# Kernel tuning notes

Hardware: AMD Instinct MI355X
Metric: run time of the kernel (lower is better)

## Reference

```python
import jax, jax.numpy as jnp
import numpy as np

S, T, D_OUT = 64, 256, 64
B = 64
HEADS = 2
D0 = S + T              # 320
D1 = D0 * (1 + HEADS)   # 960
D2 = D1 * (1 + HEADS)   # 2880
PARAM_SCALE = 0.02


def setup_inputs() -> dict:
    key = jax.random.key(0)
    k1, k2, k3, k4 = jax.random.split(key, 4)
    x = jax.random.normal(k1, (B, T, S), dtype=jnp.float32)
    A0 = jax.random.normal(k2, (HEADS, D0, D0), dtype=jnp.float32) * PARAM_SCALE
    A1 = jax.random.normal(k3, (HEADS, D1, D1), dtype=jnp.float32) * PARAM_SCALE
    Wo = jax.random.normal(k4, (D_OUT, D2), dtype=jnp.float32) * PARAM_SCALE
    return {"x": x, "A0": A0, "A1": A1, "Wo": Wo}


def _causal_self_attention(h, A):
    # h: [B, T, d], A: [H, d, d]
    Bsz, Tlen, d = h.shape
    H = A.shape[0]
    # bilinear scores per head: h @ A[i] @ h^T, vectorized over heads
    scores = jnp.einsum('btd,hde,bse->bhts', h, A, h)  # [B, H, T, T]
    neg_inf = jnp.asarray(float('-inf'), dtype=h.dtype)
    mask = jnp.triu(jnp.full((Tlen, Tlen), neg_inf, dtype=h.dtype), k=1)
    attn = jax.nn.softmax(scores + mask, axis=-1)
    out = jnp.einsum('bhts,bsd->bthd', attn, h)  # [B, T, H, d]
    return out.reshape(Bsz, Tlen, H * d)


def reference(x, A0, A1, Wo):
    Bsz, Tlen, _ = x.shape
    # one-hot positional encoding concatenated onto input
    pos = jnp.broadcast_to(jnp.eye(Tlen, dtype=x.dtype)[None], (Bsz, Tlen, Tlen))
    h = jnp.concatenate([x, pos], axis=-1)          # [B, T, S+T]
    h = jnp.concatenate([h, _causal_self_attention(h, A0)], axis=-1)  # [B, T, D1]
    h = jnp.concatenate([h, _causal_self_attention(h, A1)], axis=-1)  # [B, T, D2]
    logits = jnp.einsum('btd,od->bto', h, Wo)       # [B, T, d_out]
    return logits
```

## Files before the change

kernel.cpp:

```cpp
#include <hip/hip_runtime.h>
#include <math.h>

#define NB 64
#define NT 256
#define NS 64
#define ND0 320
#define ND1 960
#define ND2 2880
#define NH 2
#define DC 704

typedef __attribute__((ext_vector_type(8))) _Float16 f16x8;
typedef __attribute__((ext_vector_type(4))) float f32x4;
typedef __attribute__((ext_vector_type(4))) short short4v;

typedef const __attribute__((address_space(1))) void* gas_ptr;
typedef __attribute__((address_space(3))) void* las_ptr;
#define GLOAD16(g, l) __builtin_amdgcn_global_load_lds((gas_ptr)(g), (las_ptr)(l), 16, 0, 0)
#define MFMAH(a, b, c) __builtin_amdgcn_mfma_f32_16x16x32_f16((a), (b), (c), 0, 0, 0)

__device__ __forceinline__ short f2h(float v) {
    union { _Float16 h; short s; } u; u.h = (_Float16)v; return u.s;
}
__device__ __forceinline__ float h2f(short b) {
    union { _Float16 h; short s; } u; u.s = b; return (float)u.h;
}
__device__ __forceinline__ int swz(int o) { return o ^ (((o >> 7) & 7) << 4); }

__global__ __launch_bounds__(256, 2) void gemmG1(
    const short* __restrict__ hc,
    const short* __restrict__ At,
    short* __restrict__ G,
    const float* __restrict__ A1)
{
    int wg = blockIdx.x;
    int q8 = gridDim.x >> 3;
    int sid = (wg & 7) * q8 + (wg >> 3);
    int bx = sid % 15, by = sid / 15;
    int m0 = by << 8, n0 = bx << 7;

    __shared__ short lds[24576];
    int tid = threadIdx.x;
    int lane = tid & 63, w = tid >> 6;
    int wm = w >> 1, wn = w & 1;
    int q = lane >> 4, l15 = lane & 15;

    const short* aS[4]; const short* bS[2];
    int dA[4], dB[2];
#pragma unroll
    for (int j = 0; j < 4; ++j) {
        int o = j * 4096 + tid * 16;
        int c = swz(o);
        int sr = c >> 7, byt = c & 127;
        int row = sr * 2 + (byt >> 6), k = (byt & 63) >> 1;
        aS[j] = hc + (long)(m0 + row) * DC + k;
        dA[j] = o >> 1;
    }
#pragma unroll
    for (int j = 0; j < 2; ++j) {
        int o = j * 4096 + tid * 16;
        int c = swz(o);
        int sr = c >> 7, byt = c & 127;
        int row = sr * 2 + (byt >> 6), k = (byt & 63) >> 1;
        bS[j] = At + (long)(n0 + row) * DC + k;
        dB[j] = o >> 1;
    }

#define STG(BUF) { \
    GLOAD16(aS[0], lds + (BUF) + dA[0]); GLOAD16(aS[1], lds + (BUF) + dA[1]); \
    GLOAD16(aS[2], lds + (BUF) + dA[2]); GLOAD16(aS[3], lds + (BUF) + dA[3]); \
    GLOAD16(bS[0], lds + (BUF) + 8192 + dB[0]); GLOAD16(bS[1], lds + (BUF) + 8192 + dB[1]); \
    aS[0] += 32; aS[1] += 32; aS[2] += 32; aS[3] += 32; bS[0] += 32; bS[1] += 32; }

    int oa[8], ob[4];
#pragma unroll
    for (int mf = 0; mf < 8; ++mf) {
        int row = wm * 128 + mf * 16 + l15;
        int sr = row >> 1, half = row & 1;
        oa[mf] = swz(sr * 128 + half * 64 + q * 16) >> 1;
    }
#pragma unroll
    for (int nf = 0; nf < 4; ++nf) {
        int row = wn * 64 + nf * 16 + l15;
        int sr = row >> 1, half = row & 1;
        ob[nf] = swz(sr * 128 + half * 64 + q * 16) >> 1;
    }

    f32x4 acc[8][4] = {};

    STG(0)
    __syncthreads();
#pragma unroll 2
    for (int t = 0; t < 22; ++t) {
        int cur = (t & 1) * 12288;
        if (t < 21) STG(12288 - cur)
        f16x8 vb[4];
#pragma unroll
        for (int nf = 0; nf < 4; ++nf)
            vb[nf] = *(const f16x8*)(lds + cur + 8192 + ob[nf]);
#pragma unroll
        for (int mf = 0; mf < 8; ++mf) {
            f16x8 va = *(const f16x8*)(lds + cur + oa[mf]);
#pragma unroll
            for (int nf = 0; nf < 4; ++nf)
                acc[mf][nf] = MFMAH(va, vb[nf], acc[mf][nf]);
        }
        __syncthreads();
    }
#undef STG

#pragma unroll
    for (int mf = 0; mf < 8; ++mf)
#pragma unroll
        for (int nf = 0; nf < 4; ++nf) {
            int col = n0 + wn * 64 + nf * 16 + l15;
            int head = (col >= 960) ? 1 : 0;
            int colh = col - head * 960;
            const float* bA = A1 + (long)head * 921600 + colh;
            int rowb = m0 + wm * 128 + mf * 16 + (q << 2);
#pragma unroll
            for (int r = 0; r < 4; ++r) {
                int t = (rowb + r) & 255;
                float f = acc[mf][nf][r] + bA[(long)(64 + t) * 960];
                G[(long)(rowb + r) * 1920 + col] = f2h(f);
            }
        }
}

template <bool AJUMP>
__global__ __launch_bounds__(256, 3) void gemm128(
    const short* Ah, int lda, long sA,
    const short* Bh, int ldb, long sB,
    short* Sf, int ldcf, long sCf,
    const short* biasH, long ldbias,
    long hsA, long hsC,
    int K)
{
    int bx = blockIdx.x, by = blockIdx.y;
    int m0 = by * 128, n0 = bx * 128;
    if (n0 > m0 + 127) return;
    long zLo = blockIdx.z & 63, zHi = blockIdx.z >> 6;
    const short* pAh = Ah + zLo * sA + zHi * hsA;
    const short* pBh = Bh + zLo * sB;

    __shared__ short lds[16384];
    short* LAh = lds;
    short* LBh = lds + 8192;

    int tid = threadIdx.x;
    int lane = tid & 63, w = tid >> 6;
    int wr = w >> 1, wc = w & 1;

    const short* aSH[4]; const short* bSH[4];
    int aLo[4], bLo[4];
#pragma unroll
    for (int j = 0; j < 4; ++j) {
        int o = j * 4096 + tid * 16;
        int c = swz(o); int r = c >> 7, col = (c & 127) >> 1;
        aSH[j] = pAh + (long)(m0 + r) * lda + col;
        aLo[j] = o >> 1;
        bSH[j] = pBh + (long)(n0 + r) * ldb + col;
        bLo[j] = o >> 1;
    }

    int oa[4][2], ob[4][2];
#pragma unroll
    for (int mf = 0; mf < 4; ++mf)
#pragma unroll
        for (int kf = 0; kf < 2; ++kf) {
            int row = wr * 64 + mf * 16 + (lane & 15);
            oa[mf][kf] = swz(row * 128 + (kf * 32 + ((lane >> 4) << 3)) * 2) >> 1;
        }
#pragma unroll
    for (int nf = 0; nf < 4; ++nf)
#pragma unroll
        for (int kf = 0; kf < 2; ++kf) {
            int row = wc * 64 + nf * 16 + (lane & 15);
            ob[nf][kf] = swz(row * 128 + (kf * 32 + ((lane >> 4) << 3)) * 2) >> 1;
        }

    f32x4 acc[4][4] = {};

    for (int k0 = 0; k0 < K; k0 += 64) {
        int step = (AJUMP && k0 == 0) ? 320 : 64;
#pragma unroll
        for (int j = 0; j < 4; ++j) {
            GLOAD16(aSH[j], LAh + aLo[j]);
            aSH[j] += step;
            GLOAD16(bSH[j], LBh + bLo[j]);
            bSH[j] += 64;
        }
        __syncthreads();
#pragma unroll
        for (int kf = 0; kf < 2; ++kf) {
            f16x8 vbh[4];
#pragma unroll
            for (int nf = 0; nf < 4; ++nf)
                vbh[nf] = *(const f16x8*)(LBh + ob[nf][kf]);
#pragma unroll
            for (int mf = 0; mf < 4; ++mf) {
                f16x8 vah = *(const f16x8*)(LAh + oa[mf][kf]);
#pragma unroll
                for (int nf = 0; nf < 4; ++nf)
                    acc[mf][nf] = MFMAH(vah, vbh[nf], acc[mf][nf]);
            }
        }
        __syncthreads();
    }

#pragma unroll
    for (int mf = 0; mf < 4; ++mf)
#pragma unroll
        for (int nf = 0; nf < 4; ++nf) {
            f32x4 v = acc[mf][nf];
            int col  = n0 + wc * 64 + nf * 16 + (lane & 15);
            int rowb = m0 + wr * 64 + mf * 16 + ((lane >> 4) << 2);
#pragma unroll
            for (int r = 0; r < 4; ++r) {
                long o = (zLo * 256 + rowb + r) * ldbias + 64 + col + zHi * hsA;
                v[r] += h2f(biasH[o]);
            }
#pragma unroll
            for (int r = 0; r < 4; ++r)
                Sf[zLo * sCf + zHi * hsC + (long)(rowb + r) * ldcf + col] = f2h(v[r]);
        }
}

template <int BMODE, bool KCAUSAL, bool ACC, bool OUTU, bool BJUMP>
__global__ __launch_bounds__(256) void gemm_mfma(
    const short* Ah, int lda, long sA,
    const short* Bh, int ldb, long sB, long hsB,
    float* Cf, int ldcf, long sCf,
    short* Chi, int ldch, long sCh,
    const float* biasF, long ldbias, long hsBias,
    long hsA, long hsC,
    short* UThi,
    int K)
{
    int m0 = blockIdx.y * 128, n0 = blockIdx.x * 64;
    long zLo = blockIdx.z & 63, zHi = blockIdx.z >> 6;
    const short* pAh = Ah + zLo * sA + zHi * hsA;
    const short* pBh = Bh + zLo * sB + zHi * hsB;

    __shared__ short lds[12288];
    short* LAh = lds;
    short* LBh = lds + 8192;

    int tid = threadIdx.x;
    int lane = tid & 63, w = tid >> 6;
    int wr = w >> 1, wc = w & 1;

    const short* aSH[4]; const short* bSH[2];
    int aLo[4], bLo[2];
#pragma unroll
    for (int j = 0; j < 4; ++j) {
        int o = j * 4096 + tid * 16;
        int c = swz(o); int r = c >> 7, col = (c & 127) >> 1;
        aSH[j] = pAh + (long)(m0 + r) * lda + col;
        aLo[j] = o >> 1;
    }
#pragma unroll
    for (int j = 0; j < 2; ++j) {
        int o = j * 4096 + tid * 16;
        int c = swz(o); int r = c >> 7, col = (c & 127) >> 1;
        bSH[j] = pBh + (long)(n0 + r) * ldb + col;
        bLo[j] = o >> 1;
    }

    int oa[4][2], ob[2][2];
#pragma unroll
    for (int mf = 0; mf < 4; ++mf)
#pragma unroll
        for (int kf = 0; kf < 2; ++kf) {
            int row = wr * 64 + mf * 16 + (lane & 15);
            oa[mf][kf] = swz(row * 128 + (kf * 32 + ((lane >> 4) << 3)) * 2) >> 1;
        }
#pragma unroll
    for (int nf = 0; nf < 2; ++nf)
#pragma unroll
        for (int kf = 0; kf < 2; ++kf) {
            int row = wc * 32 + nf * 16 + (lane & 15);
            ob[nf][kf] = swz(row * 128 + (kf * 32 + ((lane >> 4) << 3)) * 2) >> 1;
        }

    f32x4 acc[4][2] = {};
    int Klim = KCAUSAL ? (K < m0 + 128 ? K : m0 + 128) : K;

    for (int k0 = 0; k0 < Klim; k0 += 64) {
#pragma unroll
        for (int j = 0; j < 4; ++j) {
            GLOAD16(aSH[j], LAh + aLo[j]);
            aSH[j] += 64;
        }
        long bstep = (BJUMP && k0 == 192) ? (1048576L - 192L) : 64L;
#pragma unroll
        for (int j = 0; j < 2; ++j) {
            GLOAD16(bSH[j], LBh + bLo[j]);
            bSH[j] += bstep;
        }
        __syncthreads();
#pragma unroll
        for (int kf = 0; kf < 2; ++kf) {
            f16x8 vbh[2];
#pragma unroll
            for (int nf = 0; nf < 2; ++nf)
                vbh[nf] = *(const f16x8*)(LBh + ob[nf][kf]);
#pragma unroll
            for (int mf = 0; mf < 4; ++mf) {
                f16x8 vah = *(const f16x8*)(LAh + oa[mf][kf]);
#pragma unroll
                for (int nf = 0; nf < 2; ++nf)
                    acc[mf][nf] = MFMAH(vah, vbh[nf], acc[mf][nf]);
            }
        }
        __syncthreads();
    }

#pragma unroll
    for (int mf = 0; mf < 4; ++mf)
#pragma unroll
        for (int nf = 0; nf < 2; ++nf) {
            f32x4 v = acc[mf][nf];
            int col  = n0 + wc * 32 + nf * 16 + (lane & 15);
            int rowb = m0 + wr * 64 + mf * 16 + ((lane >> 4) << 2);
            if (BMODE == 1) {
#pragma unroll
                for (int r = 0; r < 4; ++r) {
                    int t = (rowb + r) & 255;
                    v[r] += biasF[zLo * hsBias + (long)(64 + t) * ldbias + col];
                }
            } else if (BMODE == 3) {
#pragma unroll
                for (int r = 0; r < 4; ++r) {
                    int t = (rowb + r) & 255;
                    v[r] += biasF[(long)(col - n0) * 2880 + (n0 >> 6) * 960 + 64 + t];
                }
            }
            if (OUTU) {
                if (n0 == 0) {
#pragma unroll
                    for (int r = 0; r < 4; ++r)
                        Cf[(long)(rowb + r) * ldcf + col] = v[r];
                } else {
                    int head = (n0 >> 6) - 1;
                    int o = col - n0;
                    short hs[4];
#pragma unroll
                    for (int r = 0; r < 4; ++r) hs[r] = f2h(v[r]);
                    short4v th = {hs[0], hs[1], hs[2], hs[3]};
                    *(short4v*)(UThi + head * 1048576L + (long)o * 16384 + rowb) = th;
                }
            } else if (ACC) {
#pragma unroll
                for (int r = 0; r < 4; ++r)
                    Cf[zLo * sCf + (long)(rowb + r) * ldcf + col] += v[r];
            } else if (Cf) {
#pragma unroll
                for (int r = 0; r < 4; ++r)
                    Cf[zLo * sCf + (long)(rowb + r) * ldcf + col] = v[r];
            } else {
#pragma unroll
                for (int r = 0; r < 4; ++r)
                    Chi[zHi * hsC + zLo * sCh + (long)(rowb + r) * ldch + col] = f2h(v[r]);
            }
        }
}

__global__ __launch_bounds__(256) void build_all(const float* __restrict__ x,
                                                 const float* __restrict__ Wo,
                                                 const float* __restrict__ A0,
                                                 short* __restrict__ hc,
                                                 short* __restrict__ hT,
                                                 short* __restrict__ Wf,
                                                 short* __restrict__ At0) {
    __shared__ float tile[32][33];
    int blk = blockIdx.x;
    int tid = threadIdx.x;
    if (blk < 4096) {
        int idx = blk * 256 + tid;
        int bt = idx >> 6, c = idx & 63;
        hc[(long)bt * DC + c] = f2h(x[(long)bt * NS + c]);
    } else if (blk < 5120) {
        int i = blk - 4096;
        int c0 = (i & 1) * 32, t0 = ((i >> 1) & 7) * 32, b = i >> 4;
        int tx = tid & 31, ty = tid >> 5;
        const float* xb = x + (long)b * NT * NS;
#pragma unroll
        for (int ii = ty; ii < 32; ii += 8) tile[ii][tx] = xb[(long)(t0 + ii) * NS + c0 + tx];
        __syncthreads();
        long base = (long)b * (NS * 256);
#pragma unroll
        for (int ii = ty; ii < 32; ii += 8)
            hT[base + (long)(c0 + ii) * 256 + t0 + tx] = f2h(tile[tx][ii]);
    } else if (blk < 5648) {
        int idx = (blk - 5120) * 256 + tid;
        if (idx < 192 * DC) {
            int r = idx / DC, kc = idx - r * DC;
            int o = r & 63, chunk = r >> 6;
            int srck = (kc < 64) ? kc : kc + 256;
            Wf[idx] = f2h(Wo[(long)o * ND2 + chunk * 960 + srck]);
        }
    } else {
        int i = blk - 5648;
        int k0 = (i & 1) * 32;
        int n0 = ((i >> 1) % 10) * 32;
        int z  = i / 20;
        int tx = tid & 31, ty = tid >> 5;
        long hbase = (long)z * ND0 * ND0;
#pragma unroll
        for (int ii = ty; ii < 32; ii += 8)
            tile[ii][tx] = A0[hbase + (long)(k0 + ii) * ND0 + n0 + tx];
        __syncthreads();
        long obase = (long)z * ND0 * 64;
#pragma unroll
        for (int ii = ty; ii < 32; ii += 8)
            At0[obase + (long)(n0 + ii) * 64 + k0 + tx] = f2h(tile[tx][ii]);
    }
}

__global__ void build_At(const float* __restrict__ A,
                         short* __restrict__ hi,
                         int dN, int dK, int srcLd, int shift, int dSrcN) {
    __shared__ float tile[32][33];
    int k0 = blockIdx.x * 32, n0 = blockIdx.y * 32;
    long hbase = (long)blockIdx.z * srcLd * srcLd;
    int tx = threadIdx.x, ty = threadIdx.y;
#pragma unroll
    for (int i = ty; i < 32; i += 8) {
        int k = k0 + i;
        int srck = (k < 64) ? k : k + shift;
        tile[i][tx] = (n0 + tx < dSrcN) ? A[hbase + (long)srck * srcLd + n0 + tx] : 0.f;
    }
    __syncthreads();
    long obase = (long)blockIdx.z * dN * dK;
#pragma unroll
    for (int i = ty; i < 32; i += 8)
        hi[obase + (long)(n0 + i) * dK + k0 + tx] = f2h(tile[tx][i]);
}

__global__ __launch_bounds__(256) void softmax_split(const short* S,
                                                     short* pHi,
                                                     int ldo, long hs) {
    int row  = blockIdx.x * 4 + (threadIdx.x >> 6);
    int t    = row & (NT - 1);
    int hrow = row & 16383;
    int head = row >> 14;
    int lane = threadIdx.x & 63;
    int s0   = lane << 2;
    const short* p = S + (long)row * NT;

    short4v sv = *(const short4v*)(p + s0);
    float vv[4] = {h2f(sv[0]), h2f(sv[1]), h2f(sv[2]), h2f(sv[3])};
    float mx = -INFINITY;
#pragma unroll
    for (int j = 0; j < 4; ++j)
        if (s0 + j <= t) mx = fmaxf(mx, vv[j]);
    for (int off = 32; off; off >>= 1) mx = fmaxf(mx, __shfl_down(mx, off));
    mx = __shfl(mx, 0);

    float e[4]; float sum = 0.f;
#pragma unroll
    for (int j = 0; j < 4; ++j) {
        e[j] = (s0 + j <= t) ? __expf(vv[j] - mx) : 0.f;
        sum += e[j];
    }
    for (int off = 32; off; off >>= 1) sum += __shfl_down(sum, off);
    sum = __shfl(sum, 0);
    float inv = 1.f / sum;

    short hsv[4];
#pragma unroll
    for (int j = 0; j < 4; ++j) hsv[j] = f2h(e[j] * inv);
    short4v hv = {hsv[0], hsv[1], hsv[2], hsv[3]};
    *(short4v*)(pHi + (long)head * hs + (long)hrow * ldo + s0) = hv;
}

__global__ __launch_bounds__(256) void build_h0(const float* __restrict__ x,
                                                float* __restrict__ h) {
    int idx = blockIdx.x * 256 + threadIdx.x;
    int bt = idx / ND0;
    int c  = idx - bt * ND0;
    int t  = bt & (NT - 1);
    float v;
    if (c < NS) v = x[(long)bt * NS + c];
    else        v = ((c - NS) == t) ? 1.0f : 0.0f;
    h[(long)bt * ND2 + c] = v;
}

template <bool BT, bool CAUSAL>
__global__ __launch_bounds__(256) void gemm64(
    const float* __restrict__ A, int lda, long sA,
    const float* __restrict__ Bm, int ldb, long sB,
    float* __restrict__ C, int ldc, long sC, int K)
{
    int m0 = blockIdx.y * 64, n0 = blockIdx.x * 64;
    if (CAUSAL && n0 > m0 + 63) return;
    long z = blockIdx.z;
    A += z * sA; Bm += z * sB; C += z * sC;

    __shared__ float As[16][68];
    __shared__ float Bs[16][68];

    int tid = threadIdx.x;
    int tx = tid & 15, ty = tid >> 4;
    int rowA = tid >> 2, kA = (tid & 3) << 2;
    int kB = tid >> 4,  colB = (tid & 15) << 2;

    float acc[4][4] = {};

    for (int k0 = 0; k0 < K; k0 += 16) {
        float4 av = *(const float4*)(A + (long)(m0 + rowA) * lda + k0 + kA);
        As[kA + 0][rowA] = av.x; As[kA + 1][rowA] = av.y;
        As[kA + 2][rowA] = av.z; As[kA + 3][rowA] = av.w;
        if (BT) {
            float4 bv = *(const float4*)(Bm + (long)(n0 + rowA) * ldb + k0 + kA);
            Bs[kA + 0][rowA] = bv.x; Bs[kA + 1][rowA] = bv.y;
            Bs[kA + 2][rowA] = bv.z; Bs[kA + 3][rowA] = bv.w;
        } else {
            float4 bv = *(const float4*)(Bm + (long)(k0 + kB) * ldb + n0 + colB);
            *(float4*)(&Bs[kB][colB]) = bv;
        }
        __syncthreads();
#pragma unroll
        for (int kk = 0; kk < 16; ++kk) {
            float4 a4 = *(const float4*)(&As[kk][ty << 2]);
            float4 b4 = *(const float4*)(&Bs[kk][tx << 2]);
            float a[4] = {a4.x, a4.y, a4.z, a4.w};
            float b[4] = {b4.x, b4.y, b4.z, b4.w};
#pragma unroll
            for (int i = 0; i < 4; ++i)
#pragma unroll
                for (int j = 0; j < 4; ++j)
                    acc[i][j] += a[i] * b[j];
        }
        __syncthreads();
    }
#pragma unroll
    for (int i = 0; i < 4; ++i) {
        float4 v = {acc[i][0], acc[i][1], acc[i][2], acc[i][3]};
        *(float4*)(C + (long)(m0 + (ty << 2) + i) * ldc + n0 + (tx << 2)) = v;
    }
}

__global__ __launch_bounds__(256) void softmax_causal(float* __restrict__ P) {
    int row  = blockIdx.x * 4 + (threadIdx.x >> 6);
    int t    = row & (NT - 1);
    int lane = threadIdx.x & 63;
    int s0   = lane << 2;
    float* p = P + (long)row * NT;

    float4 v = *(const float4*)(p + s0);
    float vv[4] = {v.x, v.y, v.z, v.w};
    float mx = -INFINITY;
#pragma unroll
    for (int j = 0; j < 4; ++j)
        if (s0 + j <= t) mx = fmaxf(mx, vv[j]);
    for (int off = 32; off; off >>= 1) mx = fmaxf(mx, __shfl_down(mx, off));
    mx = __shfl(mx, 0);

    float e[4]; float sum = 0.f;
#pragma unroll
    for (int j = 0; j < 4; ++j) {
        e[j] = (s0 + j <= t) ? __expf(vv[j] - mx) : 0.f;
        sum += e[j];
    }
    for (int off = 32; off; off >>= 1) sum += __shfl_down(sum, off);
    sum = __shfl(sum, 0);
    float inv = 1.f / sum;
    float4 o = {e[0] * inv, e[1] * inv, e[2] * inv, e[3] * inv};
    *(float4*)(p + s0) = o;
}

extern "C" void kernel_launch(void* const* d_in, const int* in_sizes, int n_in,
                              void* d_out, int out_size, void* d_ws, size_t ws_size,
                              hipStream_t stream) {
    const float* x  = (const float*)d_in[0];
    const float* A0 = (const float*)d_in[1];
    const float* A1 = (const float*)d_in[2];
    const float* Wo = (const float*)d_in[3];
    float* out = (float*)d_out;

    if (ws_size >= 175120384UL) {
        char* wsb = (char*)d_ws;
        short* hc_hi = (short*)(wsb);
        short* G_hi  = (short*)(wsb + 46137344L);
        short* S     = (short*)(wsb + 113246208L);
        short* P     = (short*)(wsb + 146800640L);
        short* hT_hi = (short*)(wsb + 163577856L);
        short* At_hi = (short*)(wsb + 167772160L);
        short* Wf_hi = (short*)(wsb + 170655744L);
        short* UT_hi = (short*)(wsb + 170926080L);

        build_all<<<5688, 256, 0, stream>>>(x, Wo, A0, hc_hi, hT_hi, Wf_hi, At_hi);

        gemm_mfma<1, false, false, false, false><<<dim3(5, 128, 2), 256, 0, stream>>>(
            hc_hi, DC, 0L,
            At_hi, 64, 20480L, 0L,
            nullptr, 0, 0L, G_hi, 640, 320L,
            A0, 320L, 102400L,
            0L, 0L,
            nullptr, 64);
        gemm128<false><<<dim3(2, 2, 128), 256, 0, stream>>>(
            G_hi, 640, 163840L,
            hc_hi, DC, 180224L,
            S, NT, 65536L,
            G_hi, 640L,
            320L, 4194304L, 64);
        softmax_split<<<8192, 256, 0, stream>>>(S, hc_hi + 128, DC, 320L);
        gemm_mfma<0, true, false, false, false><<<dim3(1, 2, 128), 256, 0, stream>>>(
            hc_hi + 128, DC, 180224L,
            hT_hi, 256, 16384L, 0L,
            nullptr, 0, 0L,
            hc_hi + 64, DC, 180224L,
            nullptr, 0L, 0L,
            320L, 320L,
            nullptr, 256);

        gemm_mfma<3, false, false, true, false><<<dim3(3, 128, 1), 256, 0, stream>>>(
            hc_hi, DC, 0L,
            Wf_hi, DC, 0L, 0L,
            out, NS, 0L, nullptr, 0, 0L,
            Wo, 0L, 0L,
            0L, 0L,
            UT_hi, DC);

        build_At<<<dim3(22, 30, 2), dim3(32, 8), 0, stream>>>(A1, At_hi, 960, DC, ND1, 256, ND1);
        gemmG1<<<960, 256, 0, stream>>>(hc_hi, At_hi, G_hi, A1);
        gemm128<true><<<dim3(2, 2, 128), 256, 0, stream>>>(
            G_hi, 1920, 491520L,
            hc_hi, DC, 180224L,
            S, NT, 65536L,
            G_hi, 1920L,
            960L, 4194304L, DC);
        softmax_split<<<8192, 256, 0, stream>>>(S, P, 512, 256L);
        gemm_mfma<0, false, true, false, true><<<dim3(1, 2, 64), 256, 0, stream>>>(
            P, 512, 131072L,
            UT_hi, 16384, 256L, 0L,
            out, NS, 16384L, nullptr, 0, 0L,
            nullptr, 0L, 0L,
            0L, 0L,
            nullptr, 512);
        return;
    }

    float* ws = (float*)d_ws;
    float* h  = ws;
    float* G  = ws + 47185920L;
    float* Pf = ws + 47185920L + 15728640L;

    build_h0<<<(NB * NT * ND0) / 256, 256, 0, stream>>>(x, h);

    for (int layer = 0; layer < 2; ++layer) {
        int d = layer ? ND1 : ND0;
        const float* Am = layer ? A1 : A0;
        for (int head = 0; head < NH; ++head) {
            const float* Ah = Am + (long)head * d * d;
            gemm64<false, false><<<dim3(d / 64, 256, 1), 256, 0, stream>>>(
                h, ND2, 0L, Ah, d, 0L, G, d, 0L, d);
            gemm64<true, true><<<dim3(4, 4, NB), 256, 0, stream>>>(
                G, d, (long)NT * d, h, ND2, (long)NT * ND2,
                Pf, NT, (long)NT * NT, d);
            softmax_causal<<<(NB * NT) / 4, 256, 0, stream>>>(Pf);
            gemm64<false, false><<<dim3(d / 64, 4, NB), 256, 0, stream>>>(
                Pf, NT, (long)NT * NT, h, ND2, (long)NT * ND2,
                h + (long)d * (1 + head), ND2, (long)NT * ND2, NT);
        }
    }
    gemm64<true, false><<<dim3(1, 256, 1), 256, 0, stream>>>(
        h, ND2, 0L, Wo, ND2, 0L, out, NS, 0L, ND2);
}
```

Measured before the change: 172.3 us.

## Fold A1 transpose into build_all and switch gemmG1 to single-buffered BK=64

The separate build_At launch for A1 is merged into the initial build_all kernel, with a new workspace region, so one kernel launch goes away. gemmG1 changes from a double-buffered K-step of 32 to a single-buffered K-step of 64 with a new swizzled LDS layout, two MFMA k-fragments per stage and two barriers per iteration. This halves the number of loop iterations and barriers, but load latency is no longer overlapped with compute, and the workspace requirement threshold rises.

```diff
diff --git a/kernel.cpp b/kernel.cpp
--- a/kernel.cpp
+++ b/kernel.cpp
@@ -45,69 +45,63 @@
     int wm = w >> 1, wn = w & 1;
     int q = lane >> 4, l15 = lane & 15;
 
-    const short* aS[4]; const short* bS[2];
-    int dA[4], dB[2];
+    const short* aS[8]; const short* bS[4];
+    int dA[8], dB[4];
+#pragma unroll
+    for (int j = 0; j < 8; ++j) {
+        int o = j * 4096 + tid * 16;
+        int c = swz(o); int r = c >> 7, col = (c & 127) >> 1;
+        aS[j] = hc + (long)(m0 + r) * DC + col;
+        dA[j] = o >> 1;
+    }
 #pragma unroll
     for (int j = 0; j < 4; ++j) {
         int o = j * 4096 + tid * 16;
-        int c = swz(o);
-        int sr = c >> 7, byt = c & 127;
-        int row = sr * 2 + (byt >> 6), k = (byt & 63) >> 1;
-        aS[j] = hc + (long)(m0 + row) * DC + k;
-        dA[j] = o >> 1;
-    }
-#pragma unroll
-    for (int j = 0; j < 2; ++j) {
-        int o = j * 4096 + tid * 16;
-        int c = swz(o);
-        int sr = c >> 7, byt = c & 127;
-        int row = sr * 2 + (byt >> 6), k = (byt & 63) >> 1;
-        bS[j] = At + (long)(n0 + row) * DC + k;
+        int c = swz(o); int r = c >> 7, col = (c & 127) >> 1;
+        bS[j] = At + (long)(n0 + r) * DC + col;
         dB[j] = o >> 1;
     }
 
-#define STG(BUF) { \
-    GLOAD16(aS[0], lds + (BUF) + dA[0]); GLOAD16(aS[1], lds + (BUF) + dA[1]); \
-    GLOAD16(aS[2], lds + (BUF) + dA[2]); GLOAD16(aS[3], lds + (BUF) + dA[3]); \
-    GLOAD16(bS[0], lds + (BUF) + 8192 + dB[0]); GLOAD16(bS[1], lds + (BUF) + 8192 + dB[1]); \
-    aS[0] += 32; aS[1] += 32; aS[2] += 32; aS[3] += 32; bS[0] += 32; bS[1] += 32; }
-
-    int oa[8], ob[4];
-#pragma unroll
-    for (int mf = 0; mf < 8; ++mf) {
-        int row = wm * 128 + mf * 16 + l15;
-        int sr = row >> 1, half = row & 1;
-        oa[mf] = swz(sr * 128 + half * 64 + q * 16) >> 1;
-    }
-#pragma unroll
-    for (int nf = 0; nf < 4; ++nf) {
-        int row = wn * 64 + nf * 16 + l15;
-        int sr = row >> 1, half = row & 1;
-        ob[nf] = swz(sr * 128 + half * 64 + q * 16) >> 1;
-    }
+    int oa[8][2], ob[4][2];
+#pragma unroll
+    for (int mf = 0; mf < 8; ++mf)
+#pragma unroll
+        for (int kf = 0; kf < 2; ++kf) {
+            int row = wm * 128 + mf * 16 + l15;
+            oa[mf][kf] = swz(row * 128 + (kf * 32 + (q << 3)) * 2) >> 1;
+        }
+#pragma unroll
+    for (int nf = 0; nf < 4; ++nf)
+#pragma unroll
+        for (int kf = 0; kf < 2; ++kf) {
+            int row = wn * 64 + nf * 16 + l15;
+            ob[nf][kf] = swz(row * 128 + (kf * 32 + (q << 3)) * 2) >> 1;
+        }
 
     f32x4 acc[8][4] = {};
 
-    STG(0)
-    __syncthreads();
-#pragma unroll 2
-    for (int t = 0; t < 22; ++t) {
-        int cur = (t & 1) * 12288;
-        if (t < 21) STG(12288 - cur)
-        f16x8 vb[4];
-#pragma unroll
-        for (int nf = 0; nf < 4; ++nf)
-            vb[nf] = *(const f16x8*)(lds + cur + 8192 + ob[nf]);
-#pragma unroll
-        for (int mf = 0; mf < 8; ++mf) {
-            f16x8 va = *(const f16x8*)(lds + cur + oa[mf]);
+    for (int k0 = 0; k0 < DC; k0 += 64) {
+#pragma unroll
+        for (int j = 0; j < 8; ++j) { GLOAD16(aS[j], lds + dA[j]); aS[j] += 64; }
+#pragma unroll
+        for (int j = 0; j < 4; ++j) { GLOAD16(bS[j], lds + 16384 + dB[j]); bS[j] += 64; }
+        __syncthreads();
+#pragma unroll
+        for (int kf = 0; kf < 2; ++kf) {
+            f16x8 vb[4];
 #pragma unroll
             for (int nf = 0; nf < 4; ++nf)
-                acc[mf][nf] = MFMAH(va, vb[nf], acc[mf][nf]);
-        }
-        __syncthreads();
-    }
-#undef STG
+                vb[nf] = *(const f16x8*)(lds + 16384 + ob[nf][kf]);
+#pragma unroll
+            for (int mf = 0; mf < 8; ++mf) {
+                f16x8 va = *(const f16x8*)(lds + oa[mf][kf]);
+#pragma unroll
+                for (int nf = 0; nf < 4; ++nf)
+                    acc[mf][nf] = MFMAH(va, vb[nf], acc[mf][nf]);
+            }
+        }
+        __syncthreads();
+    }
 
 #pragma unroll
     for (int mf = 0; mf < 8; ++mf)
@@ -369,10 +363,12 @@
 __global__ __launch_bounds__(256) void build_all(const float* __restrict__ x,
                                                  const float* __restrict__ Wo,
                                                  const float* __restrict__ A0,
+                                                 const float* __restrict__ A1,
                                                  short* __restrict__ hc,
                                                  short* __restrict__ hT,
                                                  short* __restrict__ Wf,
-                                                 short* __restrict__ At0) {
+                                                 short* __restrict__ At0,
+                                                 short* __restrict__ At1) {
     __shared__ float tile[32][33];
     int blk = blockIdx.x;
     int tid = threadIdx.x;
@@ -400,7 +396,7 @@
             int srck = (kc < 64) ? kc : kc + 256;
             Wf[idx] = f2h(Wo[(long)o * ND2 + chunk * 960 + srck]);
         }
-    } else {
+    } else if (blk < 5688) {
         int i = blk - 5648;
         int k0 = (i & 1) * 32;
         int n0 = ((i >> 1) % 10) * 32;
@@ -415,27 +411,25 @@
 #pragma unroll
         for (int ii = ty; ii < 32; ii += 8)
             At0[obase + (long)(n0 + ii) * 64 + k0 + tx] = f2h(tile[tx][ii]);
-    }
-}
-
-__global__ void build_At(const float* __restrict__ A,
-                         short* __restrict__ hi,
-                         int dN, int dK, int srcLd, int shift, int dSrcN) {
-    __shared__ float tile[32][33];
-    int k0 = blockIdx.x * 32, n0 = blockIdx.y * 32;
-    long hbase = (long)blockIdx.z * srcLd * srcLd;
-    int tx = threadIdx.x, ty = threadIdx.y;
-#pragma unroll
-    for (int i = ty; i < 32; i += 8) {
-        int k = k0 + i;
-        int srck = (k < 64) ? k : k + shift;
-        tile[i][tx] = (n0 + tx < dSrcN) ? A[hbase + (long)srck * srcLd + n0 + tx] : 0.f;
-    }
-    __syncthreads();
-    long obase = (long)blockIdx.z * dN * dK;
-#pragma unroll
-    for (int i = ty; i < 32; i += 8)
-        hi[obase + (long)(n0 + i) * dK + k0 + tx] = f2h(tile[tx][i]);
+    } else {
+        int i = blk - 5688;
+        int k0 = (i % 22) * 32;
+        int n0 = ((i / 22) % 30) * 32;
+        int z  = i / 660;
+        int tx = tid & 31, ty = tid >> 5;
+        long hbase = (long)z * ND1 * ND1;
+#pragma unroll
+        for (int ii = ty; ii < 32; ii += 8) {
+            int k = k0 + ii;
+            int srck = (k < 64) ? k : k + 256;
+            tile[ii][tx] = A1[hbase + (long)srck * ND1 + n0 + tx];
+        }
+        __syncthreads();
+        long obase = (long)z * 960 * DC;
+#pragma unroll
+        for (int ii = ty; ii < 32; ii += 8)
+            At1[obase + (long)(n0 + ii) * DC + k0 + tx] = f2h(tile[tx][ii]);
+    }
 }
 
 __global__ __launch_bounds__(256) void softmax_split(const short* S,
@@ -580,22 +574,23 @@
     const float* Wo = (const float*)d_in[3];
     float* out = (float*)d_out;
 
-    if (ws_size >= 175120384UL) {
+    if (ws_size >= 180527104UL) {
         char* wsb = (char*)d_ws;
         short* hc_hi = (short*)(wsb);
         short* G_hi  = (short*)(wsb + 46137344L);
         short* S     = (short*)(wsb + 113246208L);
         short* P     = (short*)(wsb + 146800640L);
         short* hT_hi = (short*)(wsb + 163577856L);
-        short* At_hi = (short*)(wsb + 167772160L);
+        short* At0_h = (short*)(wsb + 167772160L);
         short* Wf_hi = (short*)(wsb + 170655744L);
         short* UT_hi = (short*)(wsb + 170926080L);
-
-        build_all<<<5688, 256, 0, stream>>>(x, Wo, A0, hc_hi, hT_hi, Wf_hi, At_hi);
+        short* At1_h = (short*)(wsb + 175120384L);
+
+        build_all<<<7008, 256, 0, stream>>>(x, Wo, A0, A1, hc_hi, hT_hi, Wf_hi, At0_h, At1_h);
 
         gemm_mfma<1, false, false, false, false><<<dim3(5, 128, 2), 256, 0, stream>>>(
             hc_hi, DC, 0L,
-            At_hi, 64, 20480L, 0L,
+            At0_h, 64, 20480L, 0L,
             nullptr, 0, 0L, G_hi, 640, 320L,
             A0, 320L, 102400L,
             0L, 0L,
@@ -624,8 +619,7 @@
             0L, 0L,
             UT_hi, DC);
 
-        build_At<<<dim3(22, 30, 2), dim3(32, 8), 0, stream>>>(A1, At_hi, 960, DC, ND1, 256, ND1);
-        gemmG1<<<960, 256, 0, stream>>>(hc_hi, At_hi, G_hi, A1);
+        gemmG1<<<960, 256, 0, stream>>>(hc_hi, At1_h, G_hi, A1);
         gemm128<true><<<dim3(2, 2, 128), 256, 0, stream>>>(
             G_hi, 1920, 491520L,
             hc_hi, DC, 180224L,
```

After: 168.2 us (median of 2 runs). 2.4% less time.
